# Optimization experiments

Measured on AMD Instinct MI355X. Metric: run time of the kernel, lower is better.

The kernel has to match this reference:

```python
import jax, jax.numpy as jnp
import numpy as np
import math

MAX_P = 150
D_MODEL = 128
N_HEADS = 4
D_HEAD = D_MODEL // N_HEADS
D_MLP = 512
D_MEM = 64
VOCAB = MAX_P + 2  # 152
EQ_TOKEN = MAX_P + 1  # 151
B = 65536


def setup_inputs() -> dict:
    key = jax.random.key(0)
    ks = jax.random.split(key, 20)
    s = 1.0 / math.sqrt(D_MODEL)
    inp = {
        "p_val": jax.random.randint(ks[0], (B,), 0, MAX_P),
        "a": jax.random.randint(ks[1], (B,), 0, MAX_P),
        "b": jax.random.randint(ks[2], (B,), 0, MAX_P),
        # embeddings
        "token_embed": jax.random.normal(ks[3], (VOCAB, D_MODEL), jnp.float32),
        "pos_embed": jax.random.normal(ks[4], (5, D_MODEL), jnp.float32),
        # TitansMemory
        "W_mem": jax.random.normal(ks[5], (D_MODEL, D_MEM), jnp.float32) * s,
        "b_mem": jnp.zeros((D_MEM,), jnp.float32),
        "W_sur": jax.random.normal(ks[6], (D_MEM, D_MODEL), jnp.float32) * (1.0 / math.sqrt(D_MEM)),
        "b_sur": jnp.zeros((D_MODEL,), jnp.float32),
        "W_m2r": jax.random.normal(ks[7], (D_MEM, D_MODEL), jnp.float32) * (1.0 / math.sqrt(D_MEM)),
        "b_m2r": jnp.zeros((D_MODEL,), jnp.float32),
        # attention
        "W_Q": jax.random.normal(ks[8], (N_HEADS, D_MODEL, D_HEAD), jnp.float32) * s,
        "W_K": jax.random.normal(ks[9], (N_HEADS, D_MODEL, D_HEAD), jnp.float32) * s,
        "W_V": jax.random.normal(ks[10], (N_HEADS, D_MODEL, D_HEAD), jnp.float32) * s,
        "W_O": jax.random.normal(ks[11], (N_HEADS, D_HEAD, D_MODEL), jnp.float32) * s,
        # MLP
        "W_mlp1": jax.random.normal(ks[12], (D_MODEL, D_MLP), jnp.float32) * s,
        "b_mlp1": jnp.zeros((D_MLP,), jnp.float32),
        "W_mlp2": jax.random.normal(ks[13], (D_MLP, D_MODEL), jnp.float32) * (1.0 / math.sqrt(D_MLP)),
        "b_mlp2": jnp.zeros((D_MODEL,), jnp.float32),
        # unembed
        "W_un": jax.random.normal(ks[14], (D_MODEL, MAX_P), jnp.float32) * s,
        "b_un": jnp.zeros((MAX_P,), jnp.float32),
    }
    return inp


def reference(p_val, a, b, token_embed, pos_embed, W_mem, b_mem, W_sur, b_sur,
              W_m2r, b_m2r, W_Q, W_K, W_V, W_O, W_mlp1, b_mlp1, W_mlp2, b_mlp2,
              W_un, b_un):
    eq = jnp.full_like(a, EQ_TOKEN)
    tokens = jnp.stack([p_val, a, b, eq], axis=1)            # [B, 4]
    x = token_embed[tokens] + pos_embed[:4][None, :, :]       # [B, 4, D]

    # Titans memory (test-time update) on the modulus token embedding
    x0 = x[:, 0, :]                                           # [B, D]
    z = jax.nn.silu(x0 @ W_mem + b_mem)                       # [B, d_mem]
    pred_x = z @ W_sur + b_sur                                # [B, D]
    update = jax.nn.silu((x0 - pred_x) @ W_mem)               # [B, d_mem]
    mem = (z + update) @ W_m2r + b_m2r                        # [B, D]
    x = x + mem[:, None, :]

    # attention
    q = jnp.einsum('bsd,hdk->bhsk', x, W_Q)
    k = jnp.einsum('bsd,hdk->bhsk', x, W_K)
    v = jnp.einsum('bsd,hdk->bhsk', x, W_V)
    scores = jnp.einsum('bhsk,bhtk->bhst', q, k) / math.sqrt(D_HEAD)
    pattern = jax.nn.softmax(scores, axis=-1)                 # [B, H, 4, 4]
    attn = jnp.einsum('bhst,bhtk->bhsk', pattern, v)
    attn = jnp.einsum('bhsk,hkm->bsm', attn, W_O)             # [B, 4, D]
    x = x + attn

    # MLP
    x = x + jax.nn.relu(x @ W_mlp1 + b_mlp1) @ W_mlp2 + b_mlp2

    # unembed the '=' position
    logits = x[:, 3, :] @ W_un + b_un                         # [B, max_p]
    return logits
```

## Files before the change

kernel.cpp:

```cpp
#include <hip/hip_runtime.h>

#define D      128
#define DM     64
#define DMLP   512
#define PMAX   150
#define VOC    152
#define EQT    151
#define NBATCH 65536

typedef __attribute__((ext_vector_type(8))) __bf16 bf16x8;
typedef __attribute__((ext_vector_type(4))) float  f32x4;

__device__ __forceinline__ float silu_f(float x){ return x / (1.0f + expf(-x)); }

#define OFF_MEMVEC 0
#define OFF_X3BASE 19200
#define OFF_KE     19328
#define OFF_KP     38784
#define OFF_SC     39296
#define OFF_O0     132896
#define OFF_O1     171296
#define OFF_O2     209696
#define OFF_O3     248096
#define OFF_M3B    248352
#define OFF_W1F    257952
#define OFF_W2F    290720
#define OFF_WUF    323488

__global__ void k_P1a(const float* __restrict__ tok, const float* __restrict__ pos,
                      const float* __restrict__ W_mem, const float* __restrict__ b_mem,
                      const float* __restrict__ W_sur, const float* __restrict__ b_sur,
                      const float* __restrict__ W_m2r, const float* __restrict__ b_m2r,
                      const float* __restrict__ W_K,
                      float* __restrict__ memvec, float* __restrict__ x3base,
                      float* __restrict__ KE, float* __restrict__ KP)
{
    int r = blockIdx.x, t = threadIdx.x;
    if (r < 150) {
        int p = r;
        __shared__ float sx0[D], sz[DM], sdiff[D], szu[DM];
        if (t < D) sx0[t] = tok[p*D + t] + pos[t];
        __syncthreads();
        if (t < DM) {
            float acc = b_mem[t];
            for (int d = 0; d < D; d++) acc += sx0[d] * W_mem[d*DM + t];
            sz[t] = silu_f(acc);
        }
        __syncthreads();
        if (t < D) {
            float acc = b_sur[t];
            for (int j = 0; j < DM; j++) acc += sz[j] * W_sur[j*D + t];
            sdiff[t] = sx0[t] - acc;
        }
        __syncthreads();
        if (t < DM) {
            float acc = 0.f;
            for (int d = 0; d < D; d++) acc += sdiff[d] * W_mem[d*DM + t];
            szu[t] = sz[t] + silu_f(acc);
        }
        __syncthreads();
        if (t < D) {
            float acc = b_m2r[t];
            for (int j = 0; j < DM; j++) acc += szu[j] * W_m2r[j*D + t];
            memvec[p*D + t] = acc;
        }
    } else if (r == 150) {
        if (t < D) x3base[t] = tok[EQT*D + t] + pos[3*D + t];
    } else {
        int idx = r - 151;
        const float* src = (idx < 152) ? (tok + idx*D) : (pos + (idx-152)*D);
        float*       dst = (idx < 152) ? (KE + idx*D)  : (KP + (idx-152)*D);
        __shared__ float s[D];
        if (t < D) s[t] = src[t];
        __syncthreads();
        if (t < D) {
            int h = t >> 5, k = t & 31;
            float acc = 0.f;
            for (int d = 0; d < D; d++) acc += s[d] * W_K[h*4096 + d*32 + k];
            dst[t] = acc;
        }
    }
}

__global__ void k_P2x(const float* __restrict__ memvec, const float* __restrict__ x3base,
                      const float* __restrict__ W_Q, const float* __restrict__ W_V,
                      const float* __restrict__ W_O,
                      const float* __restrict__ KE, const float* __restrict__ KP,
                      const float* __restrict__ tok, const float* __restrict__ pos,
                      const float* __restrict__ W1, const float* __restrict__ W2,
                      const float* __restrict__ WU,
                      float* __restrict__ SC, __bf16* __restrict__ M3B,
                      __bf16* __restrict__ O0, __bf16* __restrict__ O1,
                      __bf16* __restrict__ O2, __bf16* __restrict__ O3,
                      __bf16* __restrict__ W1f, __bf16* __restrict__ W2f, __bf16* __restrict__ WUf)
{
    int r = blockIdx.x, t = threadIdx.x;
    if (r < 300) {
        int p = r >> 1, half = r & 1;
        __shared__ float sMem[D], sIn[D], sQ3[D], sMV[D];
        if (t < D) { float m = memvec[p*D + t]; sMem[t] = m; sIn[t] = m + x3base[t]; }
        __syncthreads();
        if (t < D) {
            int h = t >> 5, k = t & 31;
            float acc = 0.f;
            for (int d = 0; d < D; d++) acc += sIn[d] * W_Q[h*4096 + d*32 + k];
            sQ3[t] = acc;
        } else {
            int c = t - D; int h = c >> 5, k = c & 31;
            float acc = 0.f;
            for (int d = 0; d < D; d++) acc += sMem[d] * W_V[h*4096 + d*32 + k];
            sMV[c] = acc;
        }
        __syncthreads();
        const float scale = 0.17677669529663687f;
        for (int ii = t; ii < 312; ii += 256) {
            int i = half*312 + ii;
            int v = i >> 2, h = i & 3;
            const float4* qh = (const float4*)(sQ3 + h*32);
            float4 s4 = {0.f, 0.f, 0.f, 0.f};
            if (v < 152) {
                const float4* ke = (const float4*)(KE + v*D + h*32);
                #pragma unroll
                for (int k = 0; k < 8; k++) {
                    float4 q = qh[k], e = ke[k];
                    s4.x += q.x*e.x; s4.y += q.y*e.y; s4.z += q.z*e.z; s4.w += q.w*e.w;
                }
            } else if (v == 152 || v == 153) {
                const float4* ke = (const float4*)(KE + ((v==152)? p : EQT)*D + h*32);
                const float4* kp = (const float4*)(KP + ((v==152)? 0 : 3)*D + h*32);
                #pragma unroll
                for (int k = 0; k < 8; k++) {
                    float4 q = qh[k], e = ke[k], pp = kp[k];
                    s4.x += q.x*(e.x+pp.x); s4.y += q.y*(e.y+pp.y);
                    s4.z += q.z*(e.z+pp.z); s4.w += q.w*(e.w+pp.w);
                }
            } else {
                const float4* kp = (const float4*)(KP + ((v==154)?1:2)*D + h*32);
                #pragma unroll
                for (int k = 0; k < 8; k++) {
                    float4 q = qh[k], pp = kp[k];
                    s4.x += q.x*pp.x; s4.y += q.y*pp.y; s4.z += q.z*pp.z; s4.w += q.w*pp.w;
                }
            }
            SC[p*624 + i] = (s4.x + s4.y + s4.z + s4.w) * scale;
        }
        if (half == 0 && t < D) {
            float acc = sIn[t];
            for (int c = 0; c < D; c++) acc += sMV[c] * W_O[c*D + t];
            M3B[p*D + t] = (__bf16)acc;
        }
        return;
    }
    int rr = r - 300;
    if (rr < 451) {
        int idx = rr;
        int tt, v; __bf16* outp;
        if (idx < 150)      { tt = 0; v = idx;       outp = O0 + v*512; }
        else if (idx < 300) { tt = 1; v = idx - 150; outp = O1 + (idx-150)*512; }
        else if (idx < 450) { tt = 2; v = idx - 300; outp = O2 + (idx-300)*512; }
        else                { tt = 3; v = EQT;       outp = O3; }
        __shared__ float sTP[D], sv[D];
        if (t < D) sTP[t] = tok[v*D + t] + pos[tt*D + t];
        __syncthreads();
        if (t < D) {
            int h = t >> 5, k = t & 31;
            float acc = 0.f;
            for (int d = 0; d < D; d++) acc += sTP[d] * W_V[h*4096 + d*32 + k];
            sv[t] = acc;
        }
        __syncthreads();
        #pragma unroll
        for (int i = 0; i < 2; i++) {
            int c = t + i*256;
            int h = c >> 7, m = c & 127;
            float acc = 0.f;
            for (int k = 0; k < 32; k++) acc += sv[h*32 + k] * W_O[h*4096 + k*128 + m];
            outp[c] = (__bf16)acc;
        }
    } else if (rr < 483) {
        int f = (rr-451)*256 + t;
        int l = f & 63, kb = (f>>6) & 3, nb = f >> 8;
        int k0 = kb*32 + (l>>4)*8, n = nb*16 + (l&15);
        #pragma unroll
        for (int j = 0; j < 8; j++) W1f[f*8 + j] = (__bf16)W1[(k0+j)*DMLP + n];
    } else if (rr < 515) {
        int f = (rr-483)*256 + t;
        int l = f & 63, g = f >> 6;
        int nb = g & 7, kb = g >> 3;
        int k0 = kb*32 + (l>>4)*8, n = nb*16 + (l&15);
        #pragma unroll
        for (int j = 0; j < 8; j++) W2f[f*8 + j] = (__bf16)W2[(k0+j)*D + n];
    } else {
        int f = (rr-515)*256 + t;
        int l = f & 63, kb = (f>>6) & 3, nb = f >> 8;
        int k0 = kb*32 + (l>>4)*8, n = nb*16 + (l&15);
        #pragma unroll
        for (int j = 0; j < 8; j++) WUf[f*8 + j] = (__bf16)((n < 150) ? WU[(k0+j)*150 + n] : 0.f);
    }
}

__global__ __launch_bounds__(256, 4) void k_fused(
    const int* __restrict__ p_val, const int* __restrict__ a_tok, const int* __restrict__ b_tok,
    const float* __restrict__ SC, const __bf16* __restrict__ O0, const __bf16* __restrict__ O1,
    const __bf16* __restrict__ O2, const __bf16* __restrict__ O3g, const __bf16* __restrict__ M3B,
    const __bf16* __restrict__ W1f, const __bf16* __restrict__ W2f, const __bf16* __restrict__ WUf,
    const float* __restrict__ b1, const float* __restrict__ b2, const float* __restrict__ bun,
    float* __restrict__ out)
{
    __shared__ __align__(16) char smem[37888];
    char* sX3 = smem + 16384;

    int tid = threadIdx.x;
    int wv = tid >> 6, l = tid & 63, lr = l & 15, quad = l >> 4;
    int tbase = blockIdx.x * 64 + wv * 16;

    const char* gW1 = (const char*)W1f;
    const char* gW2 = (const char*)W2f;

    float4 v0, v1, v2, v3;
    {
        const float4* g1 = (const float4*)gW1;
        const float4* g2 = (const float4*)gW2;
        v0 = g1[tid]; v1 = g1[tid + 256]; v2 = g2[tid]; v3 = g2[tid + 256];
    }

    {
        int s = tid >> 2, h = tid & 3;
        int gs = blockIdx.x * 64 + s;
        int p = p_val[gs], ta = a_tok[gs], tb = b_tok[gs];

        float wloc[4];
        {
            const float* SCp = SC + p*624;
            float sc0 = SCp[608 + h];
            float sc3 = SCp[612 + h];
            float sc1 = SCp[ta*4 + h] + SCp[616 + h];
            float sc2 = SCp[tb*4 + h] + SCp[620 + h];
            float mx = fmaxf(fmaxf(sc0, sc1), fmaxf(sc2, sc3));
            float e0 = expf(sc0-mx), e1 = expf(sc1-mx), e2 = expf(sc2-mx), e3 = expf(sc3-mx);
            float inv = 1.f / (e0 + e1 + e2 + e3);
            wloc[0] = e0*inv; wloc[1] = e1*inv; wloc[2] = e2*inv; wloc[3] = e3*inv;
        }
        float w[16];
        #pragma unroll
        for (int j = 0; j < 4; j++) w[h*4 + j] = wloc[j];
        #pragma unroll
        for (int m = 1; m < 4; m++) {
            int oh = h ^ m;
            #pragma unroll
            for (int j = 0; j < 4; j++) w[oh*4 + j] = __shfl_xor(wloc[j], m);
        }

        const bf16x8* m3v = (const bf16x8*)(M3B + p*128);
        const bf16x8* t0  = (const bf16x8*)(O0 + p*512);
        const bf16x8* t1  = (const bf16x8*)(O1 + ta*512);
        const bf16x8* t2  = (const bf16x8*)(O2 + tb*512);
        const bf16x8* t3  = (const bf16x8*)O3g;
        #pragma unroll
        for (int jj = 0; jj < 4; jj++) {
            int c8 = h*4 + jj;
            bf16x8 mv = m3v[c8];
            float v[8];
            #pragma unroll
            for (int e = 0; e < 8; e++) v[e] = (float)mv[e];
            #pragma unroll
            for (int hh = 0; hh < 4; hh++) {
                int o8 = hh*16 + c8;
                bf16x8 e0 = t0[o8], e1 = t1[o8], e2 = t2[o8], e3 = t3[o8];
                float w0 = w[hh*4+0], w1 = w[hh*4+1], w2 = w[hh*4+2], w3 = w[hh*4+3];
                #pragma unroll
                for (int e = 0; e < 8; e++)
                    v[e] += w0*(float)e0[e] + w1*(float)e1[e] + w2*(float)e2[e] + w3*(float)e3[e];
            }
            bf16x8 st;
            #pragma unroll
            for (int e = 0; e < 8; e++) st[e] = (__bf16)v[e];
            *(bf16x8*)(sX3 + s*256 + ((c8*16) ^ ((s&7)<<4))) = st;
        }
    }
    asm volatile("s_waitcnt lgkmcnt(0)" ::: "memory");
    __builtin_amdgcn_sched_barrier(0);

    bf16x8 a[4];
    {
        int arow = wv*16 + lr;
        #pragma unroll
        for (int kb = 0; kb < 4; kb++)
            a[kb] = *(const bf16x8*)(sX3 + arow*256 + ((kb*64 + quad*16) ^ ((lr&7)<<4)));
    }
    {
        float4* d1 = (float4*)smem;
        d1[tid] = v0; d1[tid + 256] = v1;
    }
    __syncthreads();
    {
        float4* d2 = (float4*)(smem + 16384);
        d2[tid] = v2; d2[tid + 256] = v3;
    }
    __syncthreads();

    char* sPanH = smem + 32768 + wv*1280;

    f32x4 acc2[8];
    #pragma unroll
    for (int i = 0; i < 8; i++) acc2[i] = (f32x4){0.f, 0.f, 0.f, 0.f};

    for (int cc = 0; cc < 16; cc++) {
        int p = cc & 1;
        char* w1b = smem + p*8192;
        char* w2b = smem + 16384 + p*8192;
        if (cc < 15) {
            const float4* g1 = (const float4*)(gW1 + (cc+1)*8192);
            const float4* g2 = (const float4*)(gW2 + (cc+1)*8192);
            v0 = g1[tid]; v1 = g1[tid + 256]; v2 = g2[tid]; v3 = g2[tid + 256];
        }
        #pragma unroll
        for (int nbl = 0; nbl < 2; nbl++) {
            float bv = b1[cc*32 + nbl*16 + lr];
            f32x4 acc = (f32x4){bv, bv, bv, bv};
            #pragma unroll
            for (int kb = 0; kb < 4; kb++) {
                bf16x8 w1 = *(const bf16x8*)(w1b + ((nbl*4 + kb)*64 + l)*16);
                acc = __builtin_amdgcn_mfma_f32_16x16x32_bf16(a[kb], w1, acc, 0, 0, 0);
            }
            #pragma unroll
            for (int r = 0; r < 4; r++)
                *(__bf16*)(sPanH + (((quad*4 + r)*40) + nbl*16 + lr)*2) = (__bf16)fmaxf(acc[r], 0.f);
        }
        asm volatile("s_waitcnt lgkmcnt(0)" ::: "memory");
        __builtin_amdgcn_sched_barrier(0);
        {
            bf16x8 h = *(const bf16x8*)(sPanH + (lr*40 + quad*8)*2);
            #pragma unroll
            for (int nb2 = 0; nb2 < 8; nb2++) {
                bf16x8 w2 = *(const bf16x8*)(w2b + (nb2*64 + l)*16);
                acc2[nb2] = __builtin_amdgcn_mfma_f32_16x16x32_bf16(h, w2, acc2[nb2], 0, 0, 0);
            }
        }
        if (cc < 15) {
            float4* d1 = (float4*)(smem + (p^1)*8192);
            float4* d2 = (float4*)(smem + 16384 + (p^1)*8192);
            d1[tid] = v0; d1[tid + 256] = v1; d2[tid] = v2; d2[tid + 256] = v3;
        }
        __syncthreads();
    }

    #pragma unroll
    for (int nb2 = 0; nb2 < 8; nb2++) {
        int kb = nb2 >> 1;
        bf16x8 bi;
        #pragma unroll
        for (int j = 0; j < 8; j++)
            bi[j] = (kb*32 + quad*8 + j == nb2*16 + lr) ? (__bf16)1.0f : (__bf16)0.0f;
        acc2[nb2] = __builtin_amdgcn_mfma_f32_16x16x32_bf16(a[kb], bi, acc2[nb2], 0, 0, 0);
    }

    #pragma unroll
    for (int nb2 = 0; nb2 < 8; nb2++) {
        int n = nb2*16 + lr;
        float bv = b2[n];
        #pragma unroll
        for (int r = 0; r < 4; r++) {
            float v = acc2[nb2][r] + bv;
            int row = wv*16 + quad*4 + r;
            *(__bf16*)(smem + row*256 + ((n*2) ^ ((row&7)<<4))) = (__bf16)v;
        }
    }
    asm volatile("s_waitcnt lgkmcnt(0)" ::: "memory");
    __builtin_amdgcn_sched_barrier(0);
    bf16x8 au[4];
    {
        int arow = wv*16 + lr;
        #pragma unroll
        for (int kb = 0; kb < 4; kb++)
            au[kb] = *(const bf16x8*)(smem + arow*256 + ((kb*64 + quad*16) ^ ((lr&7)<<4)));
    }

    const char* gWU = (const char*)WUf;
    char* sWU = smem + 16384;
    #pragma unroll
    for (int q = 0; q < 3; q++) {
        __syncthreads();
        if (q < 2) {
            const float4* g = (const float4*)(gWU + q*16384);
            float4 u0 = g[tid], u1 = g[tid+256], u2 = g[tid+512], u3 = g[tid+768];
            float4* dd = (float4*)sWU;
            dd[tid] = u0; dd[tid+256] = u1; dd[tid+512] = u2; dd[tid+768] = u3;
        } else {
            const float4* g = (const float4*)(gWU + 32768);
            float4 u0 = g[tid], u1 = g[tid+256];
            float4* dd = (float4*)sWU;
            dd[tid] = u0; dd[tid+256] = u1;
        }
        __syncthreads();
        int ntn = (q < 2) ? 4 : 2;
        for (int ntl = 0; ntl < ntn; ntl++) {
            int nt = q*4 + ntl;
            int n = nt*16 + lr;
            float bv = (n < 150) ? bun[n] : 0.f;
            f32x4 acc = (f32x4){bv, bv, bv, bv};
            #pragma unroll
            for (int kb = 0; kb < 4; kb++) {
                bf16x8 wu = *(const bf16x8*)(sWU + ((ntl*4 + kb)*64 + l)*16);
                acc = __builtin_amdgcn_mfma_f32_16x16x32_bf16(au[kb], wu, acc, 0, 0, 0);
            }
            if (n < 150) {
                #pragma unroll
                for (int r = 0; r < 4; r++) {
                    int rowg = tbase + quad*4 + r;
                    out[rowg*150 + n] = acc[r];
                }
            }
        }
    }
}

extern "C" void kernel_launch(void* const* d_in, const int* in_sizes, int n_in,
                              void* d_out, int out_size, void* d_ws, size_t ws_size,
                              hipStream_t stream) {
    const int*   p_val = (const int*)d_in[0];
    const int*   a_tok = (const int*)d_in[1];
    const int*   b_tok = (const int*)d_in[2];
    const float* tok   = (const float*)d_in[3];
    const float* pos   = (const float*)d_in[4];
    const float* W_mem = (const float*)d_in[5];
    const float* b_mem = (const float*)d_in[6];
    const float* W_sur = (const float*)d_in[7];
    const float* b_sur = (const float*)d_in[8];
    const float* W_m2r = (const float*)d_in[9];
    const float* b_m2r = (const float*)d_in[10];
    const float* W_Q   = (const float*)d_in[11];
    const float* W_K   = (const float*)d_in[12];
    const float* W_V   = (const float*)d_in[13];
    const float* W_O   = (const float*)d_in[14];
    const float* W1    = (const float*)d_in[15];
    const float* b1    = (const float*)d_in[16];
    const float* W2    = (const float*)d_in[17];
    const float* b2    = (const float*)d_in[18];
    const float* WU    = (const float*)d_in[19];
    const float* bun   = (const float*)d_in[20];
    float* out = (float*)d_out;

    float* ws = (float*)d_ws;
    float* memvec = ws + OFF_MEMVEC;
    float* x3base = ws + OFF_X3BASE;
    float* KE     = ws + OFF_KE;
    float* KP     = ws + OFF_KP;
    float* SC     = ws + OFF_SC;
    __bf16* O0    = (__bf16*)(ws + OFF_O0);
    __bf16* O1    = (__bf16*)(ws + OFF_O1);
    __bf16* O2    = (__bf16*)(ws + OFF_O2);
    __bf16* O3    = (__bf16*)(ws + OFF_O3);
    __bf16* M3B   = (__bf16*)(ws + OFF_M3B);
    __bf16* W1f   = (__bf16*)(ws + OFF_W1F);
    __bf16* W2f   = (__bf16*)(ws + OFF_W2F);
    __bf16* WUf   = (__bf16*)(ws + OFF_WUF);

    k_P1a<<<307, 256, 0, stream>>>(tok, pos, W_mem, b_mem, W_sur, b_sur, W_m2r, b_m2r,
                                   W_K, memvec, x3base, KE, KP);
    k_P2x<<<825, 256, 0, stream>>>(memvec, x3base, W_Q, W_V, W_O, KE, KP,
                                   tok, pos, W1, W2, WU,
                                   SC, M3B, O0, O1, O2, O3, W1f, W2f, WUf);
    k_fused<<<NBATCH/64, 256, 0, stream>>>(p_val, a_tok, b_tok, SC, O0, O1, O2, O3, M3B,
                                           W1f, W2f, WUf, b1, b2, bun, out);
}
```

Measured before the change: 173.0 us.

## Stage MLP and unembed weights into LDS via direct global-to-LDS loads

The main MLP kernel now uses global_load_lds (16-byte) to copy W1, W2 and unembed weight tiles straight into shared memory, instead of loading them into registers and storing them afterwards. This frees registers and removes the explicit LDS store step from the double-buffered loop. The b1 bias is also cached in LDS. Separately, the small precompute matvecs are split along K across all 256 threads with a shared-memory reduction, rather than leaving half the threads idle. The direct-to-LDS path depends on the compiler placing the correct vmcnt waits before the barriers.

```diff
diff --git a/kernel.cpp b/kernel.cpp
--- a/kernel.cpp
+++ b/kernel.cpp
@@ -12,6 +12,12 @@
 typedef __attribute__((ext_vector_type(4))) float  f32x4;
 
 __device__ __forceinline__ float silu_f(float x){ return x / (1.0f + expf(-x)); }
+
+__device__ __forceinline__ void gl_lds16(const void* g, void* l) {
+    __builtin_amdgcn_global_load_lds(
+        (const __attribute__((address_space(1))) void*)g,
+        (__attribute__((address_space(3))) void*)l, 16, 0, 0);
+}
 
 #define OFF_MEMVEC 0
 #define OFF_X3BASE 19200
@@ -38,47 +44,61 @@
     int r = blockIdx.x, t = threadIdx.x;
     if (r < 150) {
         int p = r;
-        __shared__ float sx0[D], sz[DM], sdiff[D], szu[DM];
+        __shared__ float sx0[D], sz[DM], sdiff[D], szu[DM], red4[4][DM], red2[2][D];
         if (t < D) sx0[t] = tok[p*D + t] + pos[t];
         __syncthreads();
-        if (t < DM) {
-            float acc = b_mem[t];
-            for (int d = 0; d < D; d++) acc += sx0[d] * W_mem[d*DM + t];
-            sz[t] = silu_f(acc);
-        }
-        __syncthreads();
-        if (t < D) {
-            float acc = b_sur[t];
-            for (int j = 0; j < DM; j++) acc += sz[j] * W_sur[j*D + t];
-            sdiff[t] = sx0[t] - acc;
-        }
-        __syncthreads();
-        if (t < DM) {
-            float acc = 0.f;
-            for (int d = 0; d < D; d++) acc += sdiff[d] * W_mem[d*DM + t];
-            szu[t] = sz[t] + silu_f(acc);
-        }
-        __syncthreads();
-        if (t < D) {
-            float acc = b_m2r[t];
-            for (int j = 0; j < DM; j++) acc += szu[j] * W_m2r[j*D + t];
-            memvec[p*D + t] = acc;
-        }
+        {
+            int out = t & 63, seg = t >> 6, k0 = seg*32;
+            float acc = 0.f;
+            for (int k = 0; k < 32; k++) acc += sx0[k0+k] * W_mem[(k0+k)*DM + out];
+            red4[seg][out] = acc;
+        }
+        __syncthreads();
+        if (t < DM) sz[t] = silu_f(b_mem[t] + red4[0][t] + red4[1][t] + red4[2][t] + red4[3][t]);
+        __syncthreads();
+        {
+            int out = t & 127, seg = t >> 7, j0 = seg*32;
+            float acc = 0.f;
+            for (int j = 0; j < 32; j++) acc += sz[j0+j] * W_sur[(j0+j)*D + out];
+            red2[seg][out] = acc;
+        }
+        __syncthreads();
+        if (t < D) sdiff[t] = sx0[t] - (b_sur[t] + red2[0][t] + red2[1][t]);
+        __syncthreads();
+        {
+            int out = t & 63, seg = t >> 6, k0 = seg*32;
+            float acc = 0.f;
+            for (int k = 0; k < 32; k++) acc += sdiff[k0+k] * W_mem[(k0+k)*DM + out];
+            red4[seg][out] = acc;
+        }
+        __syncthreads();
+        if (t < DM) szu[t] = sz[t] + silu_f(red4[0][t] + red4[1][t] + red4[2][t] + red4[3][t]);
+        __syncthreads();
+        {
+            int out = t & 127, seg = t >> 7, j0 = seg*32;
+            float acc = 0.f;
+            for (int j = 0; j < 32; j++) acc += szu[j0+j] * W_m2r[(j0+j)*D + out];
+            red2[seg][out] = acc;
+        }
+        __syncthreads();
+        if (t < D) memvec[p*D + t] = b_m2r[t] + red2[0][t] + red2[1][t];
     } else if (r == 150) {
         if (t < D) x3base[t] = tok[EQT*D + t] + pos[3*D + t];
     } else {
         int idx = r - 151;
         const float* src = (idx < 152) ? (tok + idx*D) : (pos + (idx-152)*D);
         float*       dst = (idx < 152) ? (KE + idx*D)  : (KP + (idx-152)*D);
-        __shared__ float s[D];
+        __shared__ float s[D], red2[2][D];
         if (t < D) s[t] = src[t];
         __syncthreads();
-        if (t < D) {
-            int h = t >> 5, k = t & 31;
-            float acc = 0.f;
-            for (int d = 0; d < D; d++) acc += s[d] * W_K[h*4096 + d*32 + k];
-            dst[t] = acc;
-        }
+        {
+            int out = t & 127, seg = t >> 7, h = out >> 5, kk = out & 31, d0 = seg*64;
+            float acc = 0.f;
+            for (int d = 0; d < 64; d++) acc += s[d0+d] * W_K[h*4096 + (d0+d)*32 + kk];
+            red2[seg][out] = acc;
+        }
+        __syncthreads();
+        if (t < D) dst[t] = red2[0][t] + red2[1][t];
     }
 }
 
@@ -97,7 +117,7 @@
     int r = blockIdx.x, t = threadIdx.x;
     if (r < 300) {
         int p = r >> 1, half = r & 1;
-        __shared__ float sMem[D], sIn[D], sQ3[D], sMV[D];
+        __shared__ float sMem[D], sIn[D], sQ3[D], sMV[D], redM[2][D];
         if (t < D) { float m = memvec[p*D + t]; sMem[t] = m; sIn[t] = m + x3base[t]; }
         __syncthreads();
         if (t < D) {
@@ -144,10 +164,15 @@
             }
             SC[p*624 + i] = (s4.x + s4.y + s4.z + s4.w) * scale;
         }
-        if (half == 0 && t < D) {
-            float acc = sIn[t];
-            for (int c = 0; c < D; c++) acc += sMV[c] * W_O[c*D + t];
-            M3B[p*D + t] = (__bf16)acc;
+        if (half == 0) {
+            {
+                int out = t & 127, seg = t >> 7, c0 = seg*64;
+                float acc = 0.f;
+                for (int c = 0; c < 64; c++) acc += sMV[c0+c] * W_O[(c0+c)*D + out];
+                redM[seg][out] = acc;
+            }
+            __syncthreads();
+            if (t < D) M3B[p*D + t] = (__bf16)(sIn[t] + redM[0][t] + redM[1][t]);
         }
         return;
     }
@@ -159,15 +184,17 @@
         else if (idx < 300) { tt = 1; v = idx - 150; outp = O1 + (idx-150)*512; }
         else if (idx < 450) { tt = 2; v = idx - 300; outp = O2 + (idx-300)*512; }
         else                { tt = 3; v = EQT;       outp = O3; }
-        __shared__ float sTP[D], sv[D];
+        __shared__ float sTP[D], sv[D], red2[2][D];
         if (t < D) sTP[t] = tok[v*D + t] + pos[tt*D + t];
         __syncthreads();
-        if (t < D) {
-            int h = t >> 5, k = t & 31;
-            float acc = 0.f;
-            for (int d = 0; d < D; d++) acc += sTP[d] * W_V[h*4096 + d*32 + k];
-            sv[t] = acc;
-        }
+        {
+            int out = t & 127, seg = t >> 7, h = out >> 5, kk = out & 31, d0 = seg*64;
+            float acc = 0.f;
+            for (int d = 0; d < 64; d++) acc += sTP[d0+d] * W_V[h*4096 + (d0+d)*32 + kk];
+            red2[seg][out] = acc;
+        }
+        __syncthreads();
+        if (t < D) sv[t] = red2[0][t] + red2[1][t];
         __syncthreads();
         #pragma unroll
         for (int i = 0; i < 2; i++) {
@@ -207,8 +234,9 @@
     const float* __restrict__ b1, const float* __restrict__ b2, const float* __restrict__ bun,
     float* __restrict__ out)
 {
-    __shared__ __align__(16) char smem[37888];
+    __shared__ __align__(16) char smem[39936];
     char* sX3 = smem + 16384;
+    float* sB1 = (float*)(smem + 37888);
 
     int tid = threadIdx.x;
     int wv = tid >> 6, l = tid & 63, lr = l & 15, quad = l >> 4;
@@ -217,12 +245,9 @@
     const char* gW1 = (const char*)W1f;
     const char* gW2 = (const char*)W2f;
 
-    float4 v0, v1, v2, v3;
-    {
-        const float4* g1 = (const float4*)gW1;
-        const float4* g2 = (const float4*)gW2;
-        v0 = g1[tid]; v1 = g1[tid + 256]; v2 = g2[tid]; v3 = g2[tid + 256];
-    }
+    gl_lds16(gW1 + tid*16,       smem + tid*16);
+    gl_lds16(gW1 + (tid+256)*16, smem + (tid+256)*16);
+    sB1[tid] = b1[tid]; sB1[tid+256] = b1[tid+256];
 
     {
         int s = tid >> 2, h = tid & 3;
@@ -288,15 +313,9 @@
         for (int kb = 0; kb < 4; kb++)
             a[kb] = *(const bf16x8*)(sX3 + arow*256 + ((kb*64 + quad*16) ^ ((lr&7)<<4)));
     }
-    {
-        float4* d1 = (float4*)smem;
-        d1[tid] = v0; d1[tid + 256] = v1;
-    }
     __syncthreads();
-    {
-        float4* d2 = (float4*)(smem + 16384);
-        d2[tid] = v2; d2[tid + 256] = v3;
-    }
+    gl_lds16(gW2 + tid*16,       smem + 16384 + tid*16);
+    gl_lds16(gW2 + (tid+256)*16, smem + 16384 + (tid+256)*16);
     __syncthreads();
 
     char* sPanH = smem + 32768 + wv*1280;
@@ -306,17 +325,22 @@
     for (int i = 0; i < 8; i++) acc2[i] = (f32x4){0.f, 0.f, 0.f, 0.f};
 
     for (int cc = 0; cc < 16; cc++) {
-        int p = cc & 1;
-        char* w1b = smem + p*8192;
-        char* w2b = smem + 16384 + p*8192;
+        int pb = cc & 1;
+        char* w1b = smem + pb*8192;
+        char* w2b = smem + 16384 + pb*8192;
         if (cc < 15) {
-            const float4* g1 = (const float4*)(gW1 + (cc+1)*8192);
-            const float4* g2 = (const float4*)(gW2 + (cc+1)*8192);
-            v0 = g1[tid]; v1 = g1[tid + 256]; v2 = g2[tid]; v3 = g2[tid + 256];
+            const char* g1 = gW1 + (cc+1)*8192;
+            const char* g2 = gW2 + (cc+1)*8192;
+            char* d1 = smem + (pb^1)*8192;
+            char* d2 = smem + 16384 + (pb^1)*8192;
+            gl_lds16(g1 + tid*16,       d1 + tid*16);
+            gl_lds16(g1 + (tid+256)*16, d1 + (tid+256)*16);
+            gl_lds16(g2 + tid*16,       d2 + tid*16);
+            gl_lds16(g2 + (tid+256)*16, d2 + (tid+256)*16);
         }
         #pragma unroll
         for (int nbl = 0; nbl < 2; nbl++) {
-            float bv = b1[cc*32 + nbl*16 + lr];
+            float bv = sB1[cc*32 + nbl*16 + lr];
             f32x4 acc = (f32x4){bv, bv, bv, bv};
             #pragma unroll
             for (int kb = 0; kb < 4; kb++) {
@@ -336,11 +360,6 @@
                 bf16x8 w2 = *(const bf16x8*)(w2b + (nb2*64 + l)*16);
                 acc2[nb2] = __builtin_amdgcn_mfma_f32_16x16x32_bf16(h, w2, acc2[nb2], 0, 0, 0);
             }
-        }
-        if (cc < 15) {
-            float4* d1 = (float4*)(smem + (p^1)*8192);
-            float4* d2 = (float4*)(smem + 16384 + (p^1)*8192);
-            d1[tid] = v0; d1[tid + 256] = v1; d2[tid] = v2; d2[tid + 256] = v3;
         }
         __syncthreads();
     }
@@ -382,15 +401,15 @@
     for (int q = 0; q < 3; q++) {
         __syncthreads();
         if (q < 2) {
-            const float4* g = (const float4*)(gWU + q*16384);
-            float4 u0 = g[tid], u1 = g[tid+256], u2 = g[tid+512], u3 = g[tid+768];
-            float4* dd = (float4*)sWU;
-            dd[tid] = u0; dd[tid+256] = u1; dd[tid+512] = u2; dd[tid+768] = u3;
+            const char* g = gWU + q*16384;
+            gl_lds16(g + tid*16,       sWU + tid*16);
+            gl_lds16(g + (tid+256)*16, sWU + (tid+256)*16);
+            gl_lds16(g + (tid+512)*16, sWU + (tid+512)*16);
+            gl_lds16(g + (tid+768)*16, sWU + (tid+768)*16);
         } else {
-            const float4* g = (const float4*)(gWU + 32768);
-            float4 u0 = g[tid], u1 = g[tid+256];
-            float4* dd = (float4*)sWU;
-            dd[tid] = u0; dd[tid+256] = u1;
+            const char* g = gWU + 32768;
+            gl_lds16(g + tid*16,       sWU + tid*16);
+            gl_lds16(g + (tid+256)*16, sWU + (tid+256)*16);
         }
         __syncthreads();
         int ntn = (q < 2) ? 4 : 2;
```

After: 169.4 us. 1.02x faster.
